# Kernel tuning notes

Measured on AMD Instinct MI355X. Metric: run time of the kernel, lower is better.

## Reference

```python
import jax, jax.numpy as jnp
import numpy as np

STRIDE = 4
NUM_HEADS = 8


def _make_window(x, stride, nh):
    # (B,C,H,W) -> (B, nh, S, S, (H/S)*(W/S), C/nh)
    b, c, h, w = x.shape
    x = x.reshape(b, nh, c // nh, h // stride, stride, w // stride, stride)
    x = x.transpose(0, 1, 4, 6, 3, 5, 2)
    return x.reshape(b, nh, stride, stride, (h // stride) * (w // stride), c // nh)


def _demake_window(x, h, w):
    # (B, nh, S, S, L, dh) -> (B, nh*dh, H, W)
    b, nh, s, _, L, dh = x.shape
    x = x.reshape(b, nh, s, s, h // s, w // s, dh)
    x = x.transpose(0, 1, 6, 4, 2, 5, 3)
    return x.reshape(b, nh * dh, h, w)


def _proj(x, W, bias):
    # 1x1 conv == per-pixel GEMM: (B,C,H,W),(O,C) -> (B,O,H,W)
    return jnp.einsum('bchw,oc->bohw', x, W) + bias[None, :, None, None]


def setup_inputs() -> dict:
    key = jax.random.key(0)
    ks = jax.random.split(key, 12)
    B, C, H, W = 4, 256, 64, 64
    P, V, O = 256, 256, 256  # proj/value/out channels
    inp = {
        'fea_q': jax.random.normal(ks[0], (B, C, H, W), jnp.float32),
        'fea_k': jax.random.normal(ks[1], (B, C, H, W), jnp.float32),
        'fea_v': jax.random.normal(ks[2], (B, V, H, W), jnp.float32),
        'mask_q': (jax.random.uniform(ks[3], (B, 1, H, W)) > 0.5).astype(jnp.float32),
        'mask_k': (jax.random.uniform(ks[4], (B, 1, H, W)) > 0.5).astype(jnp.float32),
        'q_w': jax.random.normal(ks[5], (P, C), jnp.float32) * 0.02,
        'q_b': jnp.zeros((P,), jnp.float32),
        'k_w': jax.random.normal(ks[6], (P, C), jnp.float32) * 0.02,
        'k_b': jnp.zeros((P,), jnp.float32),
        'v_w': jax.random.normal(ks[7], (O, V), jnp.float32) * 0.02,
        'v_b': jnp.zeros((O,), jnp.float32),
    }
    return inp


def reference(fea_q, fea_k, fea_v, mask_q, mask_k, q_w, q_b, k_w, k_b, v_w, v_b):
    B, _, H, W = fea_q.shape
    head_dim = q_w.shape[0] // NUM_HEADS
    scaling = head_dim ** (-0.5)

    query = _make_window(_proj(fea_q, q_w, q_b), STRIDE, NUM_HEADS)
    key = _make_window(_proj(fea_k, k_w, k_b), STRIDE, NUM_HEADS)
    value = _make_window(_proj(fea_v, v_w, v_b), STRIDE, NUM_HEADS)

    # (B, nh, S, S, L, L)
    weights = jnp.matmul(query, jnp.swapaxes(key, -1, -2)) * scaling

    # mask attention (no-grad in original)
    mq = _make_window(jax.lax.stop_gradient(mask_q), STRIDE, 1)
    mk = _make_window(jax.lax.stop_gradient(mask_k), STRIDE, 1)
    mask_attn = jnp.matmul(mq, jnp.swapaxes(mk, -1, -2))  # (B,1,S,S,L,L)
    mask_sum = jnp.sum(mask_attn, axis=-1, keepdims=True)
    mask_attn = mask_attn + (mask_sum == 0).astype(jnp.float32)
    mask_attn = jnp.where(mask_attn == 0, -jnp.inf,
                          jnp.where(mask_attn == 1, 0.0, mask_attn))
    weights = weights + mask_attn

    weights = jax.nn.softmax(weights, axis=-1)  # dropout p=0 -> identity
    weights = weights * (1.0 - (mask_sum == 0).astype(jnp.float32))

    out = jnp.matmul(weights, value)  # (B, nh, S, S, L, dh)
    return _demake_window(out, H, W)
```

## Files before the change

### kernel.cpp

```cpp
#include <hip/hip_runtime.h>
#include <hip/hip_bf16.h>

#define NH 8
#define DH 32
#define LW 256
#define HW 4096
#define CIN 256

typedef float f32x4 __attribute__((ext_vector_type(4)));
typedef short s16x8 __attribute__((ext_vector_type(8)));
typedef short s16x4 __attribute__((ext_vector_type(4)));

#define AS1 __attribute__((address_space(1)))
#define AS3 __attribute__((address_space(3)))

__device__ __forceinline__ short f2bf(float f) {
  __hip_bfloat16 h = __float2bfloat16(f);
  short s; __builtin_memcpy(&s, &h, 2); return s;
}

__device__ __forceinline__ void gload_lds16(const void* g, void* l) {
  __builtin_amdgcn_global_load_lds((const AS1 void*)g, (AS3 void*)l, 16, 0, 0);
}

#define KOFF 4194304
#define VOFF 8388608
#define WTOFF 12582912

__global__ void wconv_kernel(const float* __restrict__ qw, const float* __restrict__ kw,
                             const float* __restrict__ vw, short* __restrict__ ws) {
  int blk = blockIdx.x;
  int t = blk >> 5, kb = blk & 31;
  const float* W = (t == 0) ? qw : ((t == 1) ? kw : vw);
  int o = threadIdx.x;
  f32x4 w0 = *(const f32x4*)(W + o * CIN + kb * 8);
  f32x4 w1 = *(const f32x4*)(W + o * CIN + kb * 8 + 4);
  s16x8 v;
#pragma unroll
  for (int j = 0; j < 4; ++j) { v[j] = f2bf(w0[j]); v[4 + j] = f2bf(w1[j]); }
  *(s16x8*)(ws + WTOFF + (blk * 256 + o) * 8) = v;
}

__global__ void __launch_bounds__(256, 3)
proj_kernel(const float* __restrict__ fq, const float* __restrict__ fk,
            const float* __restrict__ fv,
            const float* __restrict__ qb, const float* __restrict__ kb_,
            const float* __restrict__ vb,
            short* __restrict__ ws) {
  __shared__ s16x8 SMEM[2304];

  int bid = blockIdx.x;
  int orig = (bid & 7) * 96 + (bid >> 3);
  int t = orig >> 8;
  int r0 = orig & 255;
  int b = r0 >> 6;
  int pblk = (r0 >> 1) & 31;
  int oblk = r0 & 1;

  const float* fea = (t == 0) ? fq : ((t == 1) ? fk : fv);
  const float* Bv  = (t == 0) ? qb : ((t == 1) ? kb_ : vb);
  const short* Wt  = ws + WTOFF + t * 65536;

  int p0 = pblk * 128, o0 = oblk * 128;
  int tid = threadIdx.x;
  int lane = tid & 63, wv = tid >> 6;
  int g = lane >> 4, li = lane & 15;

  const f32x4 fzero = {0.f, 0.f, 0.f, 0.f};
  f32x4 acc[2][8];
#pragma unroll
  for (int m = 0; m < 2; ++m)
#pragma unroll
    for (int n = 0; n < 8; ++n) acc[m][n] = fzero;

  const float* feab = fea + b * (CIN * HW);
  int coct = tid >> 5;
  int pq = (tid & 31) * 4;

  f32x4 ldB[8];

#define LOAD_B(cs_) do { int c0_ = (cs_) * 64; _Pragma("unroll") \
  for (int j_ = 0; j_ < 8; ++j_) \
    ldB[j_] = *(const f32x4*)(feab + (c0_ + coct * 8 + j_) * HW + p0 + pq); } while (0)

#define WRITE_B(buf_) do { _Pragma("unroll") \
  for (int pp_ = 0; pp_ < 4; ++pp_) { s16x8 v_; _Pragma("unroll") \
    for (int j_ = 0; j_ < 8; ++j_) v_[j_] = f2bf(ldB[j_][pp_]); \
    int p_ = pq + pp_; int pidx_ = p_ ^ ((p_ >> 3) & 7); \
    SMEM[(buf_) * 1024 + coct * 128 + pidx_] = v_; } } while (0)

  LOAD_B(0);
  WRITE_B(0);
  __syncthreads();

#pragma unroll
  for (int cs = 0; cs < 4; ++cs) {
    if (cs < 3) LOAD_B(cs + 1);
#pragma unroll
    for (int kk = 0; kk < 2; ++kk) {
      int kbg = cs * 8 + kk * 4 + g;
      const short* abase = Wt + (kbg * 256 + o0 + wv * 32 + li) * 8;
      s16x8 a0 = *(const s16x8*)(abase);
      s16x8 a1 = *(const s16x8*)(abase + 128);
#pragma unroll
      for (int n = 0; n < 8; ++n) {
        int p = n * 16 + li;
        int pidx = p ^ ((p >> 3) & 7);
        s16x8 bb = SMEM[(cs & 1) * 1024 + (kk * 4 + g) * 128 + pidx];
        acc[0][n] = __builtin_amdgcn_mfma_f32_16x16x32_bf16(a0, bb, acc[0][n], 0, 0, 0);
        acc[1][n] = __builtin_amdgcn_mfma_f32_16x16x32_bf16(a1, bb, acc[1][n], 0, 0, 0);
      }
    }
    if (cs < 3) {
      WRITE_B((cs + 1) & 1);
      __syncthreads();
    }
  }
#undef LOAD_B
#undef WRITE_B

  float bias_r[2][4];
#pragma unroll
  for (int m = 0; m < 2; ++m)
#pragma unroll
    for (int rr = 0; rr < 4; ++rr)
      bias_r[m][rr] = Bv[o0 + wv * 32 + m * 16 + g * 4 + rr];

  __syncthreads();
  short* Tr = (short*)SMEM;
#pragma unroll
  for (int m = 0; m < 2; ++m) {
    int ob = wv * 32 + m * 16 + g * 4;
#pragma unroll
    for (int n = 0; n < 8; ++n) {
      int p = n * 16 + li;
      s16x4 v;
#pragma unroll
      for (int rr = 0; rr < 4; ++rr) v[rr] = f2bf(acc[m][n][rr] + bias_r[m][rr]);
      *(s16x4*)(Tr + p * 136 + ob) = v;
    }
  }
  __syncthreads();

  if (t != 2) {
    short* dst = ws + (t == 0 ? 0 : KOFF);
#pragma unroll
    for (int it = 0; it < 8; ++it) {
      int c = it * 256 + tid;
      int o8 = (c >> 7) << 3;
      int pl = c & 127;
      s16x8 v = *(const s16x8*)(Tr + pl * 136 + o8);
      int pg = p0 + pl;
      int h = pg >> 6, w = pg & 63;
      int s1 = h & 3, h0 = h >> 2, s2 = w & 3, w0 = w >> 2;
      int wwin = s1 * 4 + s2, l = h0 * 16 + w0;
      int o = o0 + o8;
      int nh = o >> 5, kb = (o & 31) >> 3;
      int winbase = (b * NH + nh) * 16 + wwin;
      *(s16x8*)(dst + winbase * 8192 + (kb * 256 + l) * 8) = v;
    }
  } else {
    int d128 = tid >> 1;
    int h_idx = tid & 1;
    int o = o0 + d128;
    int nh2 = o >> 5, d = o & 31;
    int hh = (p0 >> 6) + h_idx;
    int s1e = hh & 3, h0e = hh >> 2;
#pragma unroll
    for (int j = 0; j < 8; ++j) {
      int s2e = j & 3, woct = j >> 2;
      s16x8 v;
#pragma unroll
      for (int k = 0; k < 8; ++k) {
        int pl = h_idx * 64 + s2e + 32 * woct + 4 * k;
        v[k] = Tr[pl * 136 + d128];
      }
      int wwin = s1e * 4 + s2e;
      int l_oct = h0e * 2 + woct;
      int winbase = (b * NH + nh2) * 16 + wwin;
      int idx = (l_oct >> 2) * 1024 + (l_oct & 3) * 256 + (d >> 4) * 128 + (d & 15) * 8;
      *(s16x8*)(ws + VOFF + winbase * 8192 + idx) = v;
    }
  }
}

__global__ void __launch_bounds__(256, 4)
attn_kernel(const short* __restrict__ ws, const float* __restrict__ mq,
            const float* __restrict__ mk, float* __restrict__ out) {
  __shared__ s16x8 KsV[1024];
  __shared__ s16x8 PsV[512];
  __shared__ float amaskS[256];
  __shared__ float mqS[128];
  __shared__ float facS[128];
  __shared__ int anyS[4];

  int bid = blockIdx.x;
  int orig = (bid & 7) * 128 + (bid >> 3);
  int qh = orig & 1;
  int s2 = (orig >> 1) & 3, s1 = (orig >> 3) & 3, nh = (orig >> 5) & 7, b = orig >> 8;
  int wwin = s1 * 4 + s2;
  int tid = threadIdx.x;
  int lane = tid & 63, wv = tid >> 6, g = lane >> 4, li = lane & 15;

  int winbase = (b * NH + nh) * 16 + wwin;
  const short* qt = ws + winbase * 8192;
  const short* kt = ws + KOFF + winbase * 8192;
  const short* vt = ws + VOFF + winbase * 8192;

#pragma unroll
  for (int i = 0; i < 4; ++i) {
    int seg = i * 4 + wv;
    gload_lds16(kt + (seg * 64 + lane) * 8, &KsV[seg * 64]);
  }

  {
    int l = tid;
    int h = (l >> 4) * 4 + s1, w = (l & 15) * 4 + s2;
    float mkv = mk[b * HW + h * 64 + w];
    amaskS[l] = (mkv > 0.5f) ? 0.0f : -1e30f;
    unsigned long long bal = __ballot(mkv > 0.5f);
    if (lane == 0) anyS[wv] = (bal != 0ULL) ? 1 : 0;
  }
  if (tid < 128) {
    int l = qh * 128 + tid;
    int h = (l >> 4) * 4 + s1, w = (l & 15) * 4 + s2;
    mqS[tid] = mq[b * HW + h * 64 + w];
  }

  int lq0 = wv * 32;
  s16x8 qa[2];
#pragma unroll
  for (int m = 0; m < 2; ++m)
    qa[m] = *(const s16x8*)(qt + (g * 256 + qh * 128 + lq0 + m * 16 + li) * 8);

  __syncthreads();
  int anyk = anyS[0] | anyS[1] | anyS[2] | anyS[3];

  const f32x4 fzero = {0.f, 0.f, 0.f, 0.f};
  f32x4 of[2][2];
#pragma unroll
  for (int m = 0; m < 2; ++m) { of[m][0] = fzero; of[m][1] = fzero; }
  float rs[8];
#pragma unroll
  for (int i = 0; i < 8; ++i) rs[i] = 0.0f;

  const float C = 0.17677669529663689f * 1.4426950408889634f;

#pragma unroll
  for (int lkb = 0; lkb < 4; ++lkb) {
    f32x4 sa[2][4];
#pragma unroll
    for (int n = 0; n < 4; ++n) {
      s16x8 kf = KsV[g * 256 + lkb * 64 + n * 16 + li];
#pragma unroll
      for (int m = 0; m < 2; ++m)
        sa[m][n] = __builtin_amdgcn_mfma_f32_16x16x32_bf16(qa[m], kf, fzero, 0, 0, 0);
    }
#pragma unroll
    for (int ks = 0; ks < 2; ++ks) {
#pragma unroll
      for (int n2 = 0; n2 < 2; ++n2) {
        int n = ks * 2 + n2;
        float am = amaskS[lkb * 64 + n * 16 + li];
#pragma unroll
        for (int m = 0; m < 2; ++m) {
#pragma unroll
          for (int rr = 0; rr < 4; ++rr) {
            float pval = exp2f(sa[m][n][rr] * C + am);
            rs[m * 4 + rr] += pval;
            int row = m * 16 + g * 4 + rr;
            int cl = n * 16 + li;
            int kbh = (cl >> 3) & 3;
            short* ps = (short*)&PsV[wv * 128 + kbh * 32 + row];
            ps[cl & 7] = f2bf(pval);
          }
        }
      }
      int kg = lkb * 2 + ks;
      s16x8 pb[2];
#pragma unroll
      for (int n = 0; n < 2; ++n) pb[n] = PsV[wv * 128 + g * 32 + n * 16 + li];
#pragma unroll
      for (int m2 = 0; m2 < 2; ++m2) {
        s16x8 va = *(const s16x8*)(vt + (kg * 4 + g) * 256 + m2 * 128 + li * 8);
#pragma unroll
        for (int n = 0; n < 2; ++n)
          of[m2][n] = __builtin_amdgcn_mfma_f32_16x16x32_bf16(va, pb[n], of[m2][n], 0, 0, 0);
      }
    }
  }

#pragma unroll
  for (int i = 0; i < 8; ++i) {
    float v = rs[i];
    v += __shfl_xor(v, 1);
    v += __shfl_xor(v, 2);
    v += __shfl_xor(v, 4);
    v += __shfl_xor(v, 8);
    rs[i] = v;
  }
  if (li == 0) {
#pragma unroll
    for (int m = 0; m < 2; ++m)
#pragma unroll
      for (int rr = 0; rr < 4; ++rr) {
        int row = m * 16 + g * 4 + rr;
        float sum = rs[m * 4 + rr];
        facS[wv * 32 + row] = (anyk && mqS[wv * 32 + row] > 0.5f) ? (1.0f / sum) : 0.0f;
      }
  }

#pragma unroll
  for (int m2 = 0; m2 < 2; ++m2) {
#pragma unroll
    for (int n = 0; n < 2; ++n) {
      int lloc = wv * 32 + n * 16;
      float fac = facS[lloc + li];
      int l = qh * 128 + lloc;
      int h = (l >> 4) * 4 + s1;
      int w = li * 4 + s2;
#pragma unroll
      for (int rr = 0; rr < 4; ++rr) {
        int o = nh * 32 + m2 * 16 + g * 4 + rr;
        out[((b * 256 + o) * 64 + h) * 64 + w] = of[m2][n][rr] * fac;
      }
    }
  }
}

extern "C" void kernel_launch(void* const* d_in, const int* in_sizes, int n_in,
                              void* d_out, int out_size, void* d_ws, size_t ws_size,
                              hipStream_t stream) {
  const float* fq = (const float*)d_in[0];
  const float* fk = (const float*)d_in[1];
  const float* fv = (const float*)d_in[2];
  const float* mq = (const float*)d_in[3];
  const float* mk = (const float*)d_in[4];
  const float* qw = (const float*)d_in[5];
  const float* qb = (const float*)d_in[6];
  const float* kw = (const float*)d_in[7];
  const float* kb = (const float*)d_in[8];
  const float* vw = (const float*)d_in[9];
  const float* vb = (const float*)d_in[10];
  short* ws = (short*)d_ws;

  wconv_kernel<<<96, 256, 0, stream>>>(qw, kw, vw, ws);
  proj_kernel<<<768, 256, 0, stream>>>(fq, fk, fv, qb, kb, vb, ws);
  attn_kernel<<<1024, 256, 0, stream>>>(ws, mq, mk, (float*)d_out);
}
```

Before: 48.60 us.

## Retile projection GEMM to one image row by all 256 output channels

Each projection block now covers 64 pixels (one image row) and all 256 output channels, instead of 128 pixels by 128 channels. Each feature tile is therefore converted to bf16 once per block rather than twice across two channel blocks. Each wave now keeps a 4x4 MFMA accumulator tile with A fragments preloaded per stage. The epilogue is rewritten, since every block's pixels share one window row. The trade is smaller, strided global loads per thread and more weight-fragment registers per wave.

```diff
diff --git a/kernel.cpp b/kernel.cpp
--- a/kernel.cpp
+++ b/kernel.cpp
@@ -47,47 +47,47 @@
             const float* __restrict__ qb, const float* __restrict__ kb_,
             const float* __restrict__ vb,
             short* __restrict__ ws) {
-  __shared__ s16x8 SMEM[2304];
+  __shared__ s16x8 SMEM[2112];
 
   int bid = blockIdx.x;
   int orig = (bid & 7) * 96 + (bid >> 3);
   int t = orig >> 8;
   int r0 = orig & 255;
   int b = r0 >> 6;
-  int pblk = (r0 >> 1) & 31;
-  int oblk = r0 & 1;
+  int pblk = r0 & 63;
 
   const float* fea = (t == 0) ? fq : ((t == 1) ? fk : fv);
   const float* Bv  = (t == 0) ? qb : ((t == 1) ? kb_ : vb);
   const short* Wt  = ws + WTOFF + t * 65536;
 
-  int p0 = pblk * 128, o0 = oblk * 128;
+  int p0 = pblk * 64;
   int tid = threadIdx.x;
   int lane = tid & 63, wv = tid >> 6;
   int g = lane >> 4, li = lane & 15;
 
   const f32x4 fzero = {0.f, 0.f, 0.f, 0.f};
-  f32x4 acc[2][8];
-#pragma unroll
-  for (int m = 0; m < 2; ++m)
-#pragma unroll
-    for (int n = 0; n < 8; ++n) acc[m][n] = fzero;
+  f32x4 acc[4][4];
+#pragma unroll
+  for (int m = 0; m < 4; ++m)
+#pragma unroll
+    for (int n = 0; n < 4; ++n) acc[m][n] = fzero;
 
   const float* feab = fea + b * (CIN * HW);
+  int wq = tid & 15;
+  int jh = (tid >> 4) & 1;
   int coct = tid >> 5;
-  int pq = (tid & 31) * 4;
-
-  f32x4 ldB[8];
+
+  f32x4 ldB[4];
 
 #define LOAD_B(cs_) do { int c0_ = (cs_) * 64; _Pragma("unroll") \
-  for (int j_ = 0; j_ < 8; ++j_) \
-    ldB[j_] = *(const f32x4*)(feab + (c0_ + coct * 8 + j_) * HW + p0 + pq); } while (0)
+  for (int j_ = 0; j_ < 4; ++j_) \
+    ldB[j_] = *(const f32x4*)(feab + (c0_ + coct * 8 + jh * 4 + j_) * HW + p0 + wq * 4); } while (0)
 
 #define WRITE_B(buf_) do { _Pragma("unroll") \
-  for (int pp_ = 0; pp_ < 4; ++pp_) { s16x8 v_; _Pragma("unroll") \
-    for (int j_ = 0; j_ < 8; ++j_) v_[j_] = f2bf(ldB[j_][pp_]); \
-    int p_ = pq + pp_; int pidx_ = p_ ^ ((p_ >> 3) & 7); \
-    SMEM[(buf_) * 1024 + coct * 128 + pidx_] = v_; } } while (0)
+  for (int pp_ = 0; pp_ < 4; ++pp_) { s16x4 v_; _Pragma("unroll") \
+    for (int j_ = 0; j_ < 4; ++j_) v_[j_] = f2bf(ldB[j_][pp_]); \
+    int w_ = wq * 4 + pp_; int wsw_ = w_ ^ ((w_ >> 3) & 7); \
+    *(s16x4*)((short*)SMEM + ((buf_) * 512 + coct * 64 + wsw_) * 8 + jh * 4) = v_; } } while (0)
 
   LOAD_B(0);
   WRITE_B(0);
@@ -96,19 +96,22 @@
 #pragma unroll
   for (int cs = 0; cs < 4; ++cs) {
     if (cs < 3) LOAD_B(cs + 1);
+    s16x8 aF[2][4];
+#pragma unroll
+    for (int kk = 0; kk < 2; ++kk)
+#pragma unroll
+      for (int m = 0; m < 4; ++m)
+        aF[kk][m] = *(const s16x8*)(Wt + ((cs * 8 + kk * 4 + g) * 256 + wv * 64 + m * 16 + li) * 8);
 #pragma unroll
     for (int kk = 0; kk < 2; ++kk) {
-      int kbg = cs * 8 + kk * 4 + g;
-      const short* abase = Wt + (kbg * 256 + o0 + wv * 32 + li) * 8;
-      s16x8 a0 = *(const s16x8*)(abase);
-      s16x8 a1 = *(const s16x8*)(abase + 128);
-#pragma unroll
-      for (int n = 0; n < 8; ++n) {
-        int p = n * 16 + li;
-        int pidx = p ^ ((p >> 3) & 7);
-        s16x8 bb = SMEM[(cs & 1) * 1024 + (kk * 4 + g) * 128 + pidx];
-        acc[0][n] = __builtin_amdgcn_mfma_f32_16x16x32_bf16(a0, bb, acc[0][n], 0, 0, 0);
-        acc[1][n] = __builtin_amdgcn_mfma_f32_16x16x32_bf16(a1, bb, acc[1][n], 0, 0, 0);
+#pragma unroll
+      for (int n = 0; n < 4; ++n) {
+        int w = n * 16 + li;
+        int wsw = w ^ ((w >> 3) & 7);
+        s16x8 bb = SMEM[(cs & 1) * 512 + (kk * 4 + g) * 64 + wsw];
+#pragma unroll
+        for (int m = 0; m < 4; ++m)
+          acc[m][n] = __builtin_amdgcn_mfma_f32_16x16x32_bf16(aF[kk][m], bb, acc[m][n], 0, 0, 0);
       }
     }
     if (cs < 3) {
@@ -119,66 +122,61 @@
 #undef LOAD_B
 #undef WRITE_B
 
-  float bias_r[2][4];
-#pragma unroll
-  for (int m = 0; m < 2; ++m)
-#pragma unroll
-    for (int rr = 0; rr < 4; ++rr)
-      bias_r[m][rr] = Bv[o0 + wv * 32 + m * 16 + g * 4 + rr];
+  float bias_r[4][4];
+#pragma unroll
+  for (int m = 0; m < 4; ++m) {
+    f32x4 b4 = *(const f32x4*)(Bv + wv * 64 + m * 16 + g * 4);
+#pragma unroll
+    for (int rr = 0; rr < 4; ++rr) bias_r[m][rr] = b4[rr];
+  }
 
   __syncthreads();
   short* Tr = (short*)SMEM;
 #pragma unroll
-  for (int m = 0; m < 2; ++m) {
-    int ob = wv * 32 + m * 16 + g * 4;
-#pragma unroll
-    for (int n = 0; n < 8; ++n) {
-      int p = n * 16 + li;
+  for (int m = 0; m < 4; ++m) {
+    int ob = wv * 64 + m * 16 + g * 4;
+#pragma unroll
+    for (int n = 0; n < 4; ++n) {
+      int w = n * 16 + li;
       s16x4 v;
 #pragma unroll
       for (int rr = 0; rr < 4; ++rr) v[rr] = f2bf(acc[m][n][rr] + bias_r[m][rr]);
-      *(s16x4*)(Tr + p * 136 + ob) = v;
+      *(s16x4*)(Tr + w * 264 + ob) = v;
     }
   }
   __syncthreads();
 
+  int s1 = pblk & 3, h0 = pblk >> 2;
   if (t != 2) {
     short* dst = ws + (t == 0 ? 0 : KOFF);
 #pragma unroll
     for (int it = 0; it < 8; ++it) {
-      int c = it * 256 + tid;
-      int o8 = (c >> 7) << 3;
-      int pl = c & 127;
-      s16x8 v = *(const s16x8*)(Tr + pl * 136 + o8);
-      int pg = p0 + pl;
-      int h = pg >> 6, w = pg & 63;
-      int s1 = h & 3, h0 = h >> 2, s2 = w & 3, w0 = w >> 2;
-      int wwin = s1 * 4 + s2, l = h0 * 16 + w0;
-      int o = o0 + o8;
+      int o_oct = it * 4 + (tid >> 6);
+      int w = tid & 63;
+      s16x8 v = *(const s16x8*)(Tr + w * 264 + o_oct * 8);
+      int o = o_oct * 8;
       int nh = o >> 5, kb = (o & 31) >> 3;
-      int winbase = (b * NH + nh) * 16 + wwin;
+      int s2 = w & 3, w0 = w >> 2;
+      int l = h0 * 16 + w0;
+      int winbase = (b * NH + nh) * 16 + s1 * 4 + s2;
       *(s16x8*)(dst + winbase * 8192 + (kb * 256 + l) * 8) = v;
     }
   } else {
-    int d128 = tid >> 1;
-    int h_idx = tid & 1;
-    int o = o0 + d128;
-    int nh2 = o >> 5, d = o & 31;
-    int hh = (p0 >> 6) + h_idx;
-    int s1e = hh & 3, h0e = hh >> 2;
-#pragma unroll
-    for (int j = 0; j < 8; ++j) {
-      int s2e = j & 3, woct = j >> 2;
+#pragma unroll
+    for (int it = 0; it < 8; ++it) {
+      int d = tid;
+      int s2 = it & 3, w0h = it >> 2;
+      int l_oct = h0 * 2 + w0h;
       s16x8 v;
 #pragma unroll
       for (int k = 0; k < 8; ++k) {
-        int pl = h_idx * 64 + s2e + 32 * woct + 4 * k;
-        v[k] = Tr[pl * 136 + d128];
-      }
-      int wwin = s1e * 4 + s2e;
-      int l_oct = h0e * 2 + woct;
-      int winbase = (b * NH + nh2) * 16 + wwin;
-      int idx = (l_oct >> 2) * 1024 + (l_oct & 3) * 256 + (d >> 4) * 128 + (d & 15) * 8;
+        int w = (w0h * 8 + k) * 4 + s2;
+        v[k] = Tr[w * 264 + d];
+      }
+      int dh = d & 31;
+      int nh2 = d >> 5;
+      int winbase = (b * NH + nh2) * 16 + s1 * 4 + s2;
+      int idx = l_oct * 256 + (dh >> 4) * 128 + (dh & 15) * 8;
       *(s16x8*)(ws + VOFF + winbase * 8192 + idx) = v;
     }
   }
```

After: 47.90 us (median of 3 runs). Within noise of the previous version (-1.4%).
